# Optimization experiments

Measured on AMD Instinct MI355X. Metric: run time of the kernel, lower is better.

Reference implementation:

```python
import jax, jax.numpy as jnp
import numpy as np

B, S, DIM, H, HD = 2, 2048, 512, 8, 64
VD = DIM // H  # 64
QK = H * HD


def setup_inputs() -> dict:
    key = jax.random.key(0)
    k1, k2, k3, k4, k5 = jax.random.split(key, 5)
    x = jax.random.normal(k1, (B, S, DIM), dtype=jnp.float32)
    mask = jax.random.bernoulli(k2, 0.5, (B, S))
    # per-position rotation matrices, scaled to keep activations O(1)
    rotator = jax.random.normal(k3, (B, S, HD, HD), dtype=jnp.float32) / np.sqrt(HD)
    # torch Linear weights: [out_features, in_features], no bias
    W_trans = jax.random.normal(k4, (2 * QK + DIM, DIM), dtype=jnp.float32) / np.sqrt(DIM)
    W_o = jax.random.normal(k5, (DIM, DIM), dtype=jnp.float32) / np.sqrt(DIM)
    return {"x": x, "mask": mask, "rotator": rotator, "W_trans": W_trans, "W_o": W_o}


def _taylor_attention(qs, ks, vs, mask):
    # 2nd-order Taylor approximation of exp for softmax weights
    # qs/ks: [B,S,H,HD], vs: [B,S,H,VD], mask: [B,S] key mask
    scores = jnp.einsum('bqhd,bkhd->bhqk', qs, ks) / np.sqrt(HD)
    w = 1.0 + scores + 0.5 * scores * scores
    w = jnp.where(mask[:, None, None, :], w, 0.0)
    w = w / jnp.sum(w, axis=-1, keepdims=True)
    out = jnp.einsum('bhqk,bkhd->bqhd', w, vs)
    return out.reshape(out.shape[0], out.shape[1], -1)  # [B,S,DIM]


def reference(x, mask, rotator, W_trans, W_o):
    t = x @ W_trans.T  # [B,S,2*QK+DIM]
    qs = t[..., :QK].reshape(B, S, H, HD)
    ks = t[..., QK:2 * QK].reshape(B, S, H, HD)
    vs = t[..., 2 * QK:].reshape(B, S, H, VD)
    sel = mask[..., None, None]
    qs = jnp.where(sel, jnp.einsum('bsij,bshj->bshi', rotator, qs), qs)
    ks = jnp.where(sel, jnp.einsum('bsij,bshj->bshi', rotator, ks), ks)
    out = _taylor_attention(qs, ks, vs, mask)
    return out @ W_o.T
```

## Files before the change

### kernel.cpp

```cpp
#include <hip/hip_runtime.h>
#include <hip/hip_bf16.h>

#define B_    2
#define S_    2048
#define DIM_  512
#define H_    8
#define HD_   64
#define TOUT_ 1536
#define ROWS_ (B_ * S_)

typedef unsigned short ushort_t;
typedef __attribute__((ext_vector_type(8))) __bf16 bf16x8;
typedef __attribute__((ext_vector_type(4))) float floatx4;

#define AS_GLB __attribute__((address_space(1)))
#define AS_LDS __attribute__((address_space(3)))

__device__ __forceinline__ float bf2f(unsigned int u) { return __uint_as_float(u << 16); }
__device__ __forceinline__ unsigned short f2bfu(float f) {
    unsigned u = __float_as_uint(f);
    unsigned r = (u + 0x7fffu + ((u >> 16) & 1u)) >> 16;
    return (unsigned short)r;
}

__global__ void tmha_detect(const unsigned char* mb, int* flags) {
    __shared__ int s_bf, s_f, s_u8;
    int tid = threadIdx.x;
    if (tid == 0) { s_bf = 0; s_f = 0; s_u8 = 0; }
    __syncthreads();
    int cbf = 0, cf = 0, cu8 = 0;
    for (int i = tid; i < 4096; i += 256) {
        unsigned char v = mb[i];
        if (v == 0x3F || v == 0x80) {
            cf++;
            if ((i & 3) == 1) cbf++;
        } else if (v != 0 && (i & 3) != 0) {
            cu8++;
        }
    }
    atomicAdd(&s_bf, cbf); atomicAdd(&s_f, cf); atomicAdd(&s_u8, cu8);
    __syncthreads();
    if (tid == 0) {
        int mcls;
        if (s_bf > 0)      mcls = 2;
        else if (s_f > 0)  mcls = 3;
        else if (s_u8 > 0) mcls = 0;
        else               mcls = 1;
        flags[1] = mcls;
    }
}

__global__ void tmha_decode_mask(const unsigned char* mb, const int* flags, int* wm) {
    int i = blockIdx.x * 256 + threadIdx.x;
    if (i >= ROWS_) return;
    int cls = flags[1];
    int v;
    if (cls == 0)      v = (mb[i] != 0);
    else if (cls == 1) v = (reinterpret_cast<const int*>(mb)[i] != 0);
    else if (cls == 2) v = ((reinterpret_cast<const unsigned short*>(mb)[i] & 0x7fffu) != 0);
    else               v = ((reinterpret_cast<const unsigned int*>(mb)[i] & 0x7fffffffu) != 0);
    wm[i] = v;
}

__global__ __launch_bounds__(256) void cast_bf16(const float* __restrict__ src,
                                                 ushort_t* __restrict__ dst, int n4) {
    int i = blockIdx.x * 256 + threadIdx.x;
    if (i >= n4) return;
    float4 v = reinterpret_cast<const float4*>(src)[i];
    ushort_t o[4] = {f2bfu(v.x), f2bfu(v.y), f2bfu(v.z), f2bfu(v.w)};
    reinterpret_cast<uint2*>(dst)[i] = *reinterpret_cast<uint2*>(o);
}

template <int TM, int N, int K>
__global__ __launch_bounds__(256) void mfma_gemm_bt(const ushort_t* __restrict__ A,
                                                    const ushort_t* __restrict__ Bm,
                                                    float* __restrict__ C) {
    constexpr int FM = TM / 32;
    __shared__ __align__(16) ushort_t As[TM * 64];
    __shared__ __align__(16) ushort_t Bs[128 * 64];
    int tid = threadIdx.x;
    int lane = tid & 63;
    int wv = tid >> 6;
    int wm = wv >> 1, wn = wv & 1;
    int quad = lane >> 4;
    int mrow = lane & 15;
    int bx = blockIdx.x;
    int by = blockIdx.y;

    floatx4 acc[FM][4];
#pragma unroll
    for (int i = 0; i < FM; i++)
#pragma unroll
        for (int j = 0; j < 4; j++) acc[i][j] = (floatx4){0.f, 0.f, 0.f, 0.f};

    for (int k0 = 0; k0 < K; k0 += 64) {
#pragma unroll
        for (int t = 0; t < TM / 32; t++) {
            int p = (wv * (TM / 32) + t) * 64 + lane;
            int row = p >> 3, cp = p & 7;
            int gc = cp ^ (row & 7);
            const ushort_t* ga = A + (size_t)(by * TM + row) * K + k0 + gc * 8;
            __builtin_amdgcn_global_load_lds((const AS_GLB unsigned int*)ga,
                                             (AS_LDS unsigned int*)&As[(size_t)(wv * (TM / 32) + t) * 64 * 8],
                                             16, 0, 0);
        }
#pragma unroll
        for (int t = 0; t < 4; t++) {
            int p = (wv * 4 + t) * 64 + lane;
            int row = p >> 3, cp = p & 7;
            int gc = cp ^ (row & 7);
            const ushort_t* gb = Bm + (size_t)(bx * 128 + row) * K + k0 + gc * 8;
            __builtin_amdgcn_global_load_lds((const AS_GLB unsigned int*)gb,
                                             (AS_LDS unsigned int*)&Bs[(size_t)(wv * 4 + t) * 64 * 8],
                                             16, 0, 0);
        }
        __syncthreads();
#pragma unroll
        for (int ks = 0; ks < 64; ks += 32) {
            int c = (ks >> 3) + quad;
            bf16x8 af[FM], bf[4];
#pragma unroll
            for (int i = 0; i < FM; i++) {
                int row = wm * (TM / 2) + i * 16 + mrow;
                int pos = row * 8 + (c ^ (row & 7));
                af[i] = *reinterpret_cast<const bf16x8*>(&As[pos * 8]);
            }
#pragma unroll
            for (int j = 0; j < 4; j++) {
                int row = wn * 64 + j * 16 + mrow;
                int pos = row * 8 + (c ^ (row & 7));
                bf[j] = *reinterpret_cast<const bf16x8*>(&Bs[pos * 8]);
            }
#pragma unroll
            for (int i = 0; i < FM; i++)
#pragma unroll
                for (int j = 0; j < 4; j++)
                    acc[i][j] = __builtin_amdgcn_mfma_f32_16x16x32_bf16(af[i], bf[j], acc[i][j], 0, 0, 0);
        }
        __syncthreads();
    }

    int col0 = bx * 128 + wn * 64 + mrow;
    int row0 = by * TM + wm * (TM / 2) + quad * 4;
#pragma unroll
    for (int i = 0; i < FM; i++)
#pragma unroll
        for (int j = 0; j < 4; j++)
#pragma unroll
            for (int r = 0; r < 4; r++)
                C[(size_t)(row0 + i * 16 + r) * N + col0 + j * 16] = acc[i][j][r];
}

__global__ __launch_bounds__(256) void rot_qk(const float* __restrict__ t,
                                              const float* __restrict__ rotG,
                                              const int* __restrict__ wm,
                                              ushort_t* __restrict__ Qb,
                                              ushort_t* __restrict__ Kb) {
    __shared__ float rotT[64 * 65];
    __shared__ float qk[1024];
    int row = blockIdx.x;
    int tid = threadIdx.x;
    int b = row >> 11, s = row & 2047;

    float4 mine = *reinterpret_cast<const float4*>(t + (size_t)row * TOUT_ + tid * 4);
    float out[4];

    if (wm[row]) {
        *reinterpret_cast<float4*>(&qk[tid * 4]) = mine;
        const float* rp = rotG + (size_t)row * 4096;
        for (int e = tid * 4; e < 4096; e += 1024) {
            float4 v = *reinterpret_cast<const float4*>(rp + e);
            int i = e >> 6, j = e & 63;
            rotT[(j + 0) * 65 + i] = v.x;
            rotT[(j + 1) * 65 + i] = v.y;
            rotT[(j + 2) * 65 + i] = v.z;
            rotT[(j + 3) * 65 + i] = v.w;
        }
        __syncthreads();
#pragma unroll
        for (int r = 0; r < 4; r++) {
            int u = tid * 4 + r;
            int i = u & 63;
            int base = u & ~63;
            float acc = 0.f;
            for (int j = 0; j < 64; j++) acc += rotT[j * 65 + i] * qk[base + j];
            out[r] = acc;
        }
    } else {
        out[0] = mine.x; out[1] = mine.y; out[2] = mine.z; out[3] = mine.w;
    }

    int u0 = tid * 4;
    int sel = u0 >> 9;
    int c = u0 & 511;
    int h = c >> 6, d = c & 63;
    ushort_t* dst = (sel ? Kb : Qb) + ((size_t)(b * 8 + h) * 2048 + s) * 64 + d;
    ushort_t o[4] = {f2bfu(out[0]), f2bfu(out[1]), f2bfu(out[2]), f2bfu(out[3])};
    *reinterpret_cast<uint2*>(dst) = *reinterpret_cast<uint2*>(o);
}

__global__ __launch_bounds__(256) void prep_vt(const float* __restrict__ t,
                                               const int* __restrict__ wm,
                                               ushort_t* __restrict__ VtG) {
    __shared__ float tile[64][65];
    __shared__ float mrow[64];
    int st = blockIdx.x;
    int bh = blockIdx.y;
    int b = bh >> 3, h = bh & 7;
    int tid = threadIdx.x;
    if (tid < 64) mrow[tid] = wm[b * 2048 + st * 64 + tid] ? 1.0f : 0.0f;
#pragma unroll
    for (int i = 0; i < 4; i++) {
        int q = i * 256 + tid;
        int r = q >> 4, c4 = (q & 15) * 4;
        float4 v = *reinterpret_cast<const float4*>(
            t + (size_t)(b * 2048 + st * 64 + r) * TOUT_ + 1024 + h * 64 + c4);
        tile[r][c4] = v.x; tile[r][c4 + 1] = v.y; tile[r][c4 + 2] = v.z; tile[r][c4 + 3] = v.w;
    }
    __syncthreads();
#pragma unroll
    for (int i = 0; i < 8; i++) {
        int e = i * 256 + tid;
        int d = e >> 5, sl = (e & 31) * 2;
        float v0 = tile[sl][d] * mrow[sl];
        float v1 = tile[sl + 1][d] * mrow[sl + 1];
        unsigned int u = (unsigned)f2bfu(v0) | ((unsigned)f2bfu(v1) << 16);
        *reinterpret_cast<unsigned int*>(VtG + ((size_t)bh * 65 + d) * 2048 + st * 64 + sl) = u;
    }
    if (tid < 32) {
        int sl = tid * 2;
        unsigned m0 = mrow[sl]     != 0.f ? 0x3F80u : 0u;
        unsigned m1 = mrow[sl + 1] != 0.f ? 0x3F80u : 0u;
        *reinterpret_cast<unsigned int*>(VtG + ((size_t)bh * 65 + 64) * 2048 + st * 64 + sl) = m0 | (m1 << 16);
    }
}

__global__ __launch_bounds__(256) void tmha_attn_mfma(const ushort_t* __restrict__ Qb,
                                                      const ushort_t* __restrict__ Kb,
                                                      const ushort_t* __restrict__ VtG,
                                                      ushort_t* __restrict__ attnAb) {
    __shared__ __align__(16) ushort_t Ks[1024 * 8];
    __shared__ __align__(16) ushort_t Vs[1280 * 8];
    __shared__ __align__(16) ushort_t Ps[1024 * 8];
    int tid = threadIdx.x;
    int lane = tid & 63;
    int wv = tid >> 6;
    int lm = lane & 15;
    int quad = lane >> 4;
    int qt = blockIdx.x;
    int h = blockIdx.y;
    int b = blockIdx.z;
    int bh = b * 8 + h;

    for (int i = tid; i < 960; i += 256)
        reinterpret_cast<unsigned int*>(&Vs[1040 * 8])[i] = 0u;

    bf16x8 qf[2];
    {
        const ushort_t* qp = Qb + ((size_t)bh * 2048 + qt * 64 + wv * 16 + lm) * 64 + quad * 8;
        qf[0] = *reinterpret_cast<const bf16x8*>(qp);
        qf[1] = *reinterpret_cast<const bf16x8*>(qp + 32);
    }

    floatx4 oacc[5];
#pragma unroll
    for (int j = 0; j < 5; j++) oacc[j] = (floatx4){0.f, 0.f, 0.f, 0.f};

    for (int kt = 0; kt < S_; kt += 128) {
#pragma unroll
        for (int t4 = 0; t4 < 4; t4++) {
            int p = (wv * 4 + t4) * 64 + lane;
            int row = p >> 3, cp = p & 7;
            int gc = cp ^ (row & 7);
            const ushort_t* g = Kb + ((size_t)bh * 2048 + kt + row) * 64 + gc * 8;
            __builtin_amdgcn_global_load_lds((const AS_GLB unsigned int*)g,
                                             (AS_LDS unsigned int*)&Ks[(size_t)(wv * 4 + t4) * 64 * 8],
                                             16, 0, 0);
        }
#pragma unroll
        for (int t4 = 0; t4 < 4; t4++) {
            int p = (wv * 4 + t4) * 64 + lane;
            int row = p >> 4, cp = p & 15;
            int gc = cp ^ (row & 15);
            const ushort_t* g = VtG + ((size_t)bh * 65 + row) * 2048 + kt + gc * 8;
            __builtin_amdgcn_global_load_lds((const AS_GLB unsigned int*)g,
                                             (AS_LDS unsigned int*)&Vs[(size_t)(wv * 4 + t4) * 64 * 8],
                                             16, 0, 0);
        }
        if (tid < 64) {
            unsigned int mv = *reinterpret_cast<const unsigned int*>(
                VtG + ((size_t)bh * 65 + 64) * 2048 + kt + tid * 2);
            reinterpret_cast<unsigned int*>(&Vs[1024 * 8])[tid] = mv;
        }
        __syncthreads();

        floatx4 sacc[8];
#pragma unroll
        for (int j = 0; j < 8; j++) sacc[j] = (floatx4){0.f, 0.f, 0.f, 0.f};
#pragma unroll
        for (int j = 0; j < 8; j++) {
            int row = j * 16 + lm;
#pragma unroll
            for (int kc = 0; kc < 2; kc++) {
                int c = kc * 4 + quad;
                int pos = row * 8 + (c ^ (row & 7));
                bf16x8 bk = *reinterpret_cast<const bf16x8*>(&Ks[pos * 8]);
                sacc[j] = __builtin_amdgcn_mfma_f32_16x16x32_bf16(qf[kc], bk, sacc[j], 0, 0, 0);
            }
        }

#pragma unroll
        for (int j = 0; j < 8; j++)
#pragma unroll
            for (int r = 0; r < 4; r++) {
                float s = sacc[j][r];
                float wgt = fmaf(s, fmaf(s, 0.0078125f, 0.125f), 1.0f);
                int m = wv * 16 + quad * 4 + r;
                int col = j * 16 + lm;
                int cw = col >> 3;
                int pos = m * 16 + (cw ^ (m & 15));
                Ps[pos * 8 + (col & 7)] = f2bfu(wgt);
            }
        __syncthreads();

#pragma unroll
        for (int j = 0; j < 5; j++) {
            int vrow = j * 16 + lm;
#pragma unroll
            for (int kc = 0; kc < 4; kc++) {
                int c = kc * 4 + quad;
                int ppos = (wv * 16 + lm) * 16 + (c ^ lm);
                bf16x8 pa = *reinterpret_cast<const bf16x8*>(&Ps[ppos * 8]);
                int vpos = vrow * 16 + (c ^ (vrow & 15));
                bf16x8 vb = *reinterpret_cast<const bf16x8*>(&Vs[vpos * 8]);
                oacc[j] = __builtin_amdgcn_mfma_f32_16x16x32_bf16(pa, vb, oacc[j], 0, 0, 0);
            }
        }
        __syncthreads();
    }

    float den[4];
#pragma unroll
    for (int r = 0; r < 4; r++) den[r] = __shfl(oacc[4][r], quad * 16, 64);
#pragma unroll
    for (int j = 0; j < 4; j++) {
        int col = h * 64 + j * 16 + lm;
#pragma unroll
        for (int r = 0; r < 4; r++) {
            float v = oacc[j][r] / den[r];
            attnAb[(size_t)(b * 2048 + qt * 64 + wv * 16 + quad * 4 + r) * DIM_ + col] = f2bfu(v);
        }
    }
}

extern "C" void kernel_launch(void* const* d_in, const int* in_sizes, int n_in,
                              void* d_out, int out_size, void* d_ws, size_t ws_size,
                              hipStream_t stream) {
    (void)in_sizes; (void)n_in; (void)out_size; (void)ws_size;
    const float* x    = (const float*)d_in[0];
    const void*  mask = d_in[1];
    const float* rot  = (const float*)d_in[2];
    const float* Wt   = (const float*)d_in[3];
    const float* Wo   = (const float*)d_in[4];

    char* ws = (char*)d_ws;
    int* flags       = (int*)ws;
    int* wmask       = (int*)(ws + 64);
    float* t         = (float*)(ws + 32768);
    ushort_t* Xb     = (ushort_t*)(ws + 25198592);
    ushort_t* Wtb    = (ushort_t*)(ws + 29392896);
    ushort_t* Wob    = (ushort_t*)(ws + 30965760);
    ushort_t* Qb     = (ushort_t*)(ws + 31490048);
    ushort_t* Kb     = (ushort_t*)(ws + 35684352);
    ushort_t* VtG    = (ushort_t*)(ws + 39878656);
    ushort_t* attnAb = (ushort_t*)(ws + 44138496);

    tmha_detect<<<1, 256, 0, stream>>>((const unsigned char*)mask, flags);
    tmha_decode_mask<<<16, 256, 0, stream>>>((const unsigned char*)mask, flags, wmask);

    cast_bf16<<<(ROWS_ * DIM_ / 4 + 255) / 256, 256, 0, stream>>>(x, Xb, ROWS_ * DIM_ / 4);
    cast_bf16<<<(TOUT_ * DIM_ / 4 + 255) / 256, 256, 0, stream>>>(Wt, Wtb, TOUT_ * DIM_ / 4);
    cast_bf16<<<(DIM_ * DIM_ / 4 + 255) / 256, 256, 0, stream>>>(Wo, Wob, DIM_ * DIM_ / 4);

    {
        dim3 grid(TOUT_ / 128, ROWS_ / 64);
        mfma_gemm_bt<64, TOUT_, DIM_><<<grid, 256, 0, stream>>>(Xb, Wtb, t);
    }

    rot_qk<<<ROWS_, 256, 0, stream>>>(t, rot, wmask, Qb, Kb);

    {
        dim3 grid(32, 16);
        prep_vt<<<grid, 256, 0, stream>>>(t, wmask, VtG);
    }

    {
        dim3 grid(32, 8, 2);
        tmha_attn_mfma<<<grid, 256, 0, stream>>>(Qb, Kb, VtG, attnAb);
    }

    {
        dim3 grid(DIM_ / 128, ROWS_ / 64);
        mfma_gemm_bt<64, DIM_, DIM_><<<grid, 256, 0, stream>>>(attnAb, Wob, (float*)d_out);
    }
}
```

Before: 207.7 us.

## Use MFMA for per-row rotation and give each attention wave two query tiles

The per-position rotation of Q/K moves from an LDS-transposed scalar FMA loop to bf16 MFMA, with one wave per row and all 16 head vectors handled as a 16x64 by 64x64 product. This drops the LDS transpose and the block-wide barrier. The attention kernel moves to 128 threads where each wave covers 32 query rows, so every K/V fragment read from LDS feeds two MFMAs. In exchange there are fewer waves per block, so less latency hiding, plus more registers per thread. The rotation matrix and Q/K are now rounded to bf16 before the rotation rather than after it, which lowers precision.

```diff
diff --git a/kernel.cpp b/kernel.cpp
--- a/kernel.cpp
+++ b/kernel.cpp
@@ -21,6 +21,13 @@
     unsigned u = __float_as_uint(f);
     unsigned r = (u + 0x7fffu + ((u >> 16) & 1u)) >> 16;
     return (unsigned short)r;
+}
+__device__ __forceinline__ bf16x8 cvt8(const float* p) {
+    float4 a = *reinterpret_cast<const float4*>(p);
+    float4 b = *reinterpret_cast<const float4*>(p + 4);
+    ushort_t o[8] = {f2bfu(a.x), f2bfu(a.y), f2bfu(a.z), f2bfu(a.w),
+                     f2bfu(b.x), f2bfu(b.y), f2bfu(b.z), f2bfu(b.w)};
+    return *reinterpret_cast<bf16x8*>(o);
 }
 
 __global__ void tmha_detect(const unsigned char* mb, int* flags) {
@@ -151,52 +158,56 @@
                 C[(size_t)(row0 + i * 16 + r) * N + col0 + j * 16] = acc[i][j][r];
 }
 
-__global__ __launch_bounds__(256) void rot_qk(const float* __restrict__ t,
-                                              const float* __restrict__ rotG,
-                                              const int* __restrict__ wm,
-                                              ushort_t* __restrict__ Qb,
-                                              ushort_t* __restrict__ Kb) {
-    __shared__ float rotT[64 * 65];
-    __shared__ float qk[1024];
-    int row = blockIdx.x;
-    int tid = threadIdx.x;
+__global__ __launch_bounds__(256) void rot_qk_mfma(const float* __restrict__ t,
+                                                   const float* __restrict__ rotG,
+                                                   const int* __restrict__ wm,
+                                                   ushort_t* __restrict__ Qb,
+                                                   ushort_t* __restrict__ Kb) {
+    int lane = threadIdx.x & 63;
+    int wv = threadIdx.x >> 6;
+    int row = blockIdx.x * 4 + wv;
     int b = row >> 11, s = row & 2047;
-
-    float4 mine = *reinterpret_cast<const float4*>(t + (size_t)row * TOUT_ + tid * 4);
-    float out[4];
+    int lm = lane & 15, quad = lane >> 4;
+    const float* trow = t + (size_t)row * TOUT_;
 
     if (wm[row]) {
-        *reinterpret_cast<float4*>(&qk[tid * 4]) = mine;
-        const float* rp = rotG + (size_t)row * 4096;
-        for (int e = tid * 4; e < 4096; e += 1024) {
-            float4 v = *reinterpret_cast<const float4*>(rp + e);
-            int i = e >> 6, j = e & 63;
-            rotT[(j + 0) * 65 + i] = v.x;
-            rotT[(j + 1) * 65 + i] = v.y;
-            rotT[(j + 2) * 65 + i] = v.z;
-            rotT[(j + 3) * 65 + i] = v.w;
-        }
-        __syncthreads();
-#pragma unroll
-        for (int r = 0; r < 4; r++) {
-            int u = tid * 4 + r;
-            int i = u & 63;
-            int base = u & ~63;
-            float acc = 0.f;
-            for (int j = 0; j < 64; j++) acc += rotT[j * 65 + i] * qk[base + j];
-            out[r] = acc;
-        }
+        bf16x8 af[2];
+#pragma unroll
+        for (int kc = 0; kc < 2; kc++)
+            af[kc] = cvt8(trow + lm * 64 + kc * 32 + quad * 8);
+
+        const float* R = rotG + (size_t)row * 4096;
+        floatx4 dacc[4];
+#pragma unroll
+        for (int nb = 0; nb < 4; nb++) dacc[nb] = (floatx4){0.f, 0.f, 0.f, 0.f};
+#pragma unroll
+        for (int nb = 0; nb < 4; nb++)
+#pragma unroll
+            for (int kc = 0; kc < 2; kc++) {
+                bf16x8 bfr = cvt8(R + (size_t)(nb * 16 + lm) * 64 + kc * 32 + quad * 8);
+                dacc[nb] = __builtin_amdgcn_mfma_f32_16x16x32_bf16(af[kc], bfr, dacc[nb], 0, 0, 0);
+            }
+#pragma unroll
+        for (int nb = 0; nb < 4; nb++)
+#pragma unroll
+            for (int r = 0; r < 4; r++) {
+                int vec = quad * 4 + r;
+                int h = vec & 7;
+                ushort_t* dst = (vec >= 8 ? Kb : Qb);
+                dst[((size_t)(b * 8 + h) * 2048 + s) * 64 + nb * 16 + lm] = f2bfu(dacc[nb][r]);
+            }
     } else {
-        out[0] = mine.x; out[1] = mine.y; out[2] = mine.z; out[3] = mine.w;
-    }
-
-    int u0 = tid * 4;
-    int sel = u0 >> 9;
-    int c = u0 & 511;
-    int h = c >> 6, d = c & 63;
-    ushort_t* dst = (sel ? Kb : Qb) + ((size_t)(b * 8 + h) * 2048 + s) * 64 + d;
-    ushort_t o[4] = {f2bfu(out[0]), f2bfu(out[1]), f2bfu(out[2]), f2bfu(out[3])};
-    *reinterpret_cast<uint2*>(dst) = *reinterpret_cast<uint2*>(o);
+#pragma unroll
+        for (int nb = 0; nb < 4; nb++)
+#pragma unroll
+            for (int r = 0; r < 4; r++) {
+                int vec = quad * 4 + r;
+                int h = vec & 7;
+                float v = trow[vec * 64 + nb * 16 + lm];
+                ushort_t* dst = (vec >= 8 ? Kb : Qb);
+                dst[((size_t)(b * 8 + h) * 2048 + s) * 64 + nb * 16 + lm] = f2bfu(v);
+            }
+    }
 }
 
 __global__ __launch_bounds__(256) void prep_vt(const float* __restrict__ t,
@@ -235,7 +246,7 @@
     }
 }
 
-__global__ __launch_bounds__(256) void tmha_attn_mfma(const ushort_t* __restrict__ Qb,
+__global__ __launch_bounds__(128) void tmha_attn_mfma(const ushort_t* __restrict__ Qb,
                                                       const ushort_t* __restrict__ Kb,
                                                       const ushort_t* __restrict__ VtG,
                                                       ushort_t* __restrict__ attnAb) {
@@ -252,39 +263,42 @@
     int b = blockIdx.z;
     int bh = b * 8 + h;
 
-    for (int i = tid; i < 960; i += 256)
+    for (int i = tid; i < 960; i += 128)
         reinterpret_cast<unsigned int*>(&Vs[1040 * 8])[i] = 0u;
 
-    bf16x8 qf[2];
-    {
-        const ushort_t* qp = Qb + ((size_t)bh * 2048 + qt * 64 + wv * 16 + lm) * 64 + quad * 8;
-        qf[0] = *reinterpret_cast<const bf16x8*>(qp);
-        qf[1] = *reinterpret_cast<const bf16x8*>(qp + 32);
-    }
-
-    floatx4 oacc[5];
-#pragma unroll
-    for (int j = 0; j < 5; j++) oacc[j] = (floatx4){0.f, 0.f, 0.f, 0.f};
+    bf16x8 qf[2][2];
+#pragma unroll
+    for (int mi = 0; mi < 2; mi++) {
+        const ushort_t* qp = Qb + ((size_t)bh * 2048 + qt * 64 + wv * 32 + mi * 16 + lm) * 64 + quad * 8;
+        qf[mi][0] = *reinterpret_cast<const bf16x8*>(qp);
+        qf[mi][1] = *reinterpret_cast<const bf16x8*>(qp + 32);
+    }
+
+    floatx4 oacc[2][5];
+#pragma unroll
+    for (int mi = 0; mi < 2; mi++)
+#pragma unroll
+        for (int j = 0; j < 5; j++) oacc[mi][j] = (floatx4){0.f, 0.f, 0.f, 0.f};
 
     for (int kt = 0; kt < S_; kt += 128) {
 #pragma unroll
-        for (int t4 = 0; t4 < 4; t4++) {
-            int p = (wv * 4 + t4) * 64 + lane;
+        for (int t4 = 0; t4 < 8; t4++) {
+            int p = (wv * 8 + t4) * 64 + lane;
             int row = p >> 3, cp = p & 7;
             int gc = cp ^ (row & 7);
             const ushort_t* g = Kb + ((size_t)bh * 2048 + kt + row) * 64 + gc * 8;
             __builtin_amdgcn_global_load_lds((const AS_GLB unsigned int*)g,
-                                             (AS_LDS unsigned int*)&Ks[(size_t)(wv * 4 + t4) * 64 * 8],
+                                             (AS_LDS unsigned int*)&Ks[(size_t)(wv * 8 + t4) * 64 * 8],
                                              16, 0, 0);
         }
 #pragma unroll
-        for (int t4 = 0; t4 < 4; t4++) {
-            int p = (wv * 4 + t4) * 64 + lane;
+        for (int t4 = 0; t4 < 8; t4++) {
+            int p = (wv * 8 + t4) * 64 + lane;
             int row = p >> 4, cp = p & 15;
             int gc = cp ^ (row & 15);
             const ushort_t* g = VtG + ((size_t)bh * 65 + row) * 2048 + kt + gc * 8;
             __builtin_amdgcn_global_load_lds((const AS_GLB unsigned int*)g,
-                                             (AS_LDS unsigned int*)&Vs[(size_t)(wv * 4 + t4) * 64 * 8],
+                                             (AS_LDS unsigned int*)&Vs[(size_t)(wv * 8 + t4) * 64 * 8],
                                              16, 0, 0);
         }
         if (tid < 64) {
@@ -294,9 +308,11 @@
         }
         __syncthreads();
 
-        floatx4 sacc[8];
-#pragma unroll
-        for (int j = 0; j < 8; j++) sacc[j] = (floatx4){0.f, 0.f, 0.f, 0.f};
+        floatx4 sacc[2][8];
+#pragma unroll
+        for (int mi = 0; mi < 2; mi++)
+#pragma unroll
+            for (int j = 0; j < 8; j++) sacc[mi][j] = (floatx4){0.f, 0.f, 0.f, 0.f};
 #pragma unroll
         for (int j = 0; j < 8; j++) {
             int row = j * 16 + lm;
@@ -305,50 +321,62 @@
                 int c = kc * 4 + quad;
                 int pos = row * 8 + (c ^ (row & 7));
                 bf16x8 bk = *reinterpret_cast<const bf16x8*>(&Ks[pos * 8]);
-                sacc[j] = __builtin_amdgcn_mfma_f32_16x16x32_bf16(qf[kc], bk, sacc[j], 0, 0, 0);
-            }
-        }
-
-#pragma unroll
-        for (int j = 0; j < 8; j++)
-#pragma unroll
-            for (int r = 0; r < 4; r++) {
-                float s = sacc[j][r];
-                float wgt = fmaf(s, fmaf(s, 0.0078125f, 0.125f), 1.0f);
-                int m = wv * 16 + quad * 4 + r;
-                int col = j * 16 + lm;
-                int cw = col >> 3;
-                int pos = m * 16 + (cw ^ (m & 15));
-                Ps[pos * 8 + (col & 7)] = f2bfu(wgt);
-            }
+                sacc[0][j] = __builtin_amdgcn_mfma_f32_16x16x32_bf16(qf[0][kc], bk, sacc[0][j], 0, 0, 0);
+                sacc[1][j] = __builtin_amdgcn_mfma_f32_16x16x32_bf16(qf[1][kc], bk, sacc[1][j], 0, 0, 0);
+            }
+        }
+
+#pragma unroll
+        for (int mi = 0; mi < 2; mi++)
+#pragma unroll
+            for (int j = 0; j < 8; j++)
+#pragma unroll
+                for (int r = 0; r < 4; r++) {
+                    float s = sacc[mi][j][r];
+                    float wgt = fmaf(s, fmaf(s, 0.0078125f, 0.125f), 1.0f);
+                    int m = wv * 32 + mi * 16 + quad * 4 + r;
+                    int col = j * 16 + lm;
+                    int cw = col >> 3;
+                    int pos = m * 16 + (cw ^ (m & 15));
+                    Ps[pos * 8 + (col & 7)] = f2bfu(wgt);
+                }
         __syncthreads();
 
 #pragma unroll
-        for (int j = 0; j < 5; j++) {
-            int vrow = j * 16 + lm;
-#pragma unroll
-            for (int kc = 0; kc < 4; kc++) {
-                int c = kc * 4 + quad;
-                int ppos = (wv * 16 + lm) * 16 + (c ^ lm);
-                bf16x8 pa = *reinterpret_cast<const bf16x8*>(&Ps[ppos * 8]);
+        for (int kc = 0; kc < 4; kc++) {
+            int c = kc * 4 + quad;
+            bf16x8 pa[2];
+#pragma unroll
+            for (int mi = 0; mi < 2; mi++) {
+                int row = wv * 32 + mi * 16 + lm;
+                int pos = row * 16 + (c ^ (row & 15));
+                pa[mi] = *reinterpret_cast<const bf16x8*>(&Ps[pos * 8]);
+            }
+#pragma unroll
+            for (int j = 0; j < 5; j++) {
+                int vrow = j * 16 + lm;
                 int vpos = vrow * 16 + (c ^ (vrow & 15));
                 bf16x8 vb = *reinterpret_cast<const bf16x8*>(&Vs[vpos * 8]);
-                oacc[j] = __builtin_amdgcn_mfma_f32_16x16x32_bf16(pa, vb, oacc[j], 0, 0, 0);
+                oacc[0][j] = __builtin_amdgcn_mfma_f32_16x16x32_bf16(pa[0], vb, oacc[0][j], 0, 0, 0);
+                oacc[1][j] = __builtin_amdgcn_mfma_f32_16x16x32_bf16(pa[1], vb, oacc[1][j], 0, 0, 0);
             }
         }
         __syncthreads();
     }
 
-    float den[4];
-#pragma unroll
-    for (int r = 0; r < 4; r++) den[r] = __shfl(oacc[4][r], quad * 16, 64);
-#pragma unroll
-    for (int j = 0; j < 4; j++) {
-        int col = h * 64 + j * 16 + lm;
-#pragma unroll
-        for (int r = 0; r < 4; r++) {
-            float v = oacc[j][r] / den[r];
-            attnAb[(size_t)(b * 2048 + qt * 64 + wv * 16 + quad * 4 + r) * DIM_ + col] = f2bfu(v);
+#pragma unroll
+    for (int mi = 0; mi < 2; mi++) {
+        float den[4];
+#pragma unroll
+        for (int r = 0; r < 4; r++) den[r] = __shfl(oacc[mi][4][r], quad * 16, 64);
+#pragma unroll
+        for (int j = 0; j < 4; j++) {
+            int col = h * 64 + j * 16 + lm;
+#pragma unroll
+            for (int r = 0; r < 4; r++) {
+                float v = oacc[mi][j][r] / den[r];
+                attnAb[(size_t)(b * 2048 + qt * 64 + wv * 32 + mi * 16 + quad * 4 + r) * DIM_ + col] = f2bfu(v);
+            }
         }
     }
 }
@@ -387,7 +415,7 @@
         mfma_gemm_bt<64, TOUT_, DIM_><<<grid, 256, 0, stream>>>(Xb, Wtb, t);
     }
 
-    rot_qk<<<ROWS_, 256, 0, stream>>>(t, rot, wmask, Qb, Kb);
+    rot_qk_mfma<<<ROWS_ / 4, 256, 0, stream>>>(t, rot, wmask, Qb, Kb);
 
     {
         dim3 grid(32, 16);
@@ -396,7 +424,7 @@
 
     {
         dim3 grid(32, 8, 2);
-        tmha_attn_mfma<<<grid, 256, 0, stream>>>(Qb, Kb, VtG, attnAb);
+        tmha_attn_mfma<<<grid, 128, 0, stream>>>(Qb, Kb, VtG, attnAb);
     }
 
     {
```

Result: no change. 204.2 us (-1.7%).
